# Optimization experiments

Measured on AMD Instinct MI355X. Metric: run time of the kernel, lower is better.

## Reference

```python
import jax, jax.numpy as jnp
import numpy as np

N_NODES = 10000
W_DIM = 512
N_EDGES = 200000


def setup_inputs() -> dict:
    key = jax.random.key(0)
    k1, k2, k3 = jax.random.split(key, 3)
    z_drug = jax.random.normal(k1, (N_NODES, W_DIM), dtype=jnp.float32)
    # glorot-style init for the bilinear weight
    glorot_std = jnp.sqrt(2.0 / (W_DIM + W_DIM)).astype(jnp.float32)
    weight = jax.random.normal(k2, (W_DIM, W_DIM), dtype=jnp.float32) * glorot_std
    batch_edges = jax.random.randint(k3, (2, N_EDGES), 0, N_NODES, dtype=jnp.int64)
    return {"z_drug": z_drug, "weight": weight, "batch_edges": batch_edges}


def reference(z_drug, weight, batch_edges):
    # edge_type == 'drug_drug': both endpoints come from the drug table.
    row_embed = z_drug[batch_edges[0]]  # [E, d]
    col_embed = z_drug[batch_edges[1]]  # [E, d]
    # score_e = row_e @ W @ col_e  == diag((Z1 W) Z2^T) without the N x N blowup
    score = jnp.einsum('ed,df,ef->e', row_embed, weight, col_embed)
    return jax.nn.sigmoid(score)  # is_sigmoid=True default
```

## Files before the change

kernel.cpp:

```cpp
#include <hip/hip_runtime.h>
#include <math.h>

#define DIM     512
#define NNODES  10000
#define NEDGES  200000
#define MPAD    10048
#define NMB     157
#define NGRP    5
#define NB      (NGRP * NNODES)
#define SCAN_BLK 49

using short8  = __attribute__((ext_vector_type(8))) short;
using floatx4 = __attribute__((ext_vector_type(4))) float;
using half8   = __attribute__((ext_vector_type(8))) _Float16;
using half2v  = __attribute__((ext_vector_type(2))) _Float16;

__device__ inline float dot2acc(half2v a, half2v b, float c) {
#if __has_builtin(__builtin_amdgcn_fdot2)
    return __builtin_amdgcn_fdot2(a, b, c, false);
#else
    return fmaf((float)a[0], (float)b[0], fmaf((float)a[1], (float)b[1], c));
#endif
}

#define PREP_ZBLK 2512
__global__ __launch_bounds__(256) void prep(const float* __restrict__ Z,
                                            const float* __restrict__ W,
                                            _Float16* __restrict__ Zh16,
                                            _Float16* __restrict__ Wh16t,
                                            int* __restrict__ counts) {
    const int b = blockIdx.x;
    const int t = threadIdx.x;

    if (b < 196) {
        int i = b * 256 + t;
        if (i < NB) counts[i] = 0;
    }

    if (b < PREP_ZBLK) {
        const int idx8 = (b * 256 + t) * 8;
        const int m = idx8 >> 9;
        float x[8];
        if (m < NNODES) {
            float4 v0 = *(const float4*)(Z + idx8);
            float4 v1 = *(const float4*)(Z + idx8 + 4);
            x[0]=v0.x; x[1]=v0.y; x[2]=v0.z; x[3]=v0.w;
            x[4]=v1.x; x[5]=v1.y; x[6]=v1.z; x[7]=v1.w;
        } else {
            #pragma unroll
            for (int j = 0; j < 8; ++j) x[j] = 0.f;
        }
        half8 h;
        #pragma unroll
        for (int j = 0; j < 8; ++j) h[j] = (_Float16)x[j];
        *(half8*)(Zh16 + idx8) = h;
    } else {
        __shared__ float tile[64][65];
        const int wb = b - PREP_ZBLK;
        const int kb = (wb >> 3) * 64;
        const int nb = (wb & 7) * 64;
        const int kk = t >> 2;
        const int ch = t & 3;

        const float* src = W + (size_t)(kb + kk) * DIM + nb + ch * 16;
        #pragma unroll
        for (int q = 0; q < 4; ++q) {
            float4 v = *(const float4*)(src + q * 4);
            tile[kk][ch * 16 + q * 4 + 0] = v.x;
            tile[kk][ch * 16 + q * 4 + 1] = v.y;
            tile[kk][ch * 16 + q * 4 + 2] = v.z;
            tile[kk][ch * 16 + q * 4 + 3] = v.w;
        }
        __syncthreads();

        const int nn = kk;
        half8 h0, h1;
        #pragma unroll
        for (int i = 0; i < 8; ++i) h0[i] = (_Float16)tile[ch * 16 + i][nn];
        #pragma unroll
        for (int i = 0; i < 8; ++i) h1[i] = (_Float16)tile[ch * 16 + 8 + i][nn];
        _Float16* d = Wh16t + (size_t)(nb + nn) * DIM + kb + ch * 16;
        *(half8*)(d)     = h0;
        *(half8*)(d + 8) = h1;
    }
}

__global__ __launch_bounds__(256) void gemm_f16(const _Float16* __restrict__ Zh16,
                                                const _Float16* __restrict__ Wh16t,
                                                _Float16* __restrict__ ZWh) {
    __shared__ _Float16 Abuf[2][64 * 32];
    __shared__ _Float16 Bbuf[2][128 * 32];

    const int t     = threadIdx.x;
    const int bid   = blockIdx.x;
    const int n_idx = bid & 3;
    const int m0    = (bid >> 2) * 64;
    const int n0    = n_idx * 128;

    const int l  = t & 63;
    const int w  = t >> 6;
    const int wn = w * 32;
    const int lm = l & 15;
    const int lq = l >> 4;
    const unsigned wbase = (unsigned)(t & 192);

    floatx4 acc[4][2] = {};

    const int arow = t >> 2;
    const int ach  = t & 3;

    auto stage = [&](int buf, int k0) {
        {
            const _Float16* s = Zh16 + (size_t)(m0 + arow) * DIM + k0 + ach * 8;
            __builtin_amdgcn_global_load_lds(
                (const __attribute__((address_space(1))) void*)s,
                (__attribute__((address_space(3))) void*)&Abuf[buf][wbase * 8], 16, 0, 0);
        }
        #pragma unroll
        for (int p = 0; p < 2; ++p) {
            const int sidx = p * 256 + t;
            const int row  = sidx >> 2;
            const int ch   = sidx & 3;
            const _Float16* s = Wh16t + (size_t)(n0 + row) * DIM + k0 + ch * 8;
            __builtin_amdgcn_global_load_lds(
                (const __attribute__((address_space(1))) void*)s,
                (__attribute__((address_space(3))) void*)&Bbuf[buf][(p * 256 + wbase) * 8], 16, 0, 0);
        }
    };

    stage(0, 0);
    __syncthreads();

    for (int s = 0; s < 16; ++s) {
        const int buf = s & 1;
        if (s < 15) stage(buf ^ 1, (s + 1) * 32);

        half8 aF[4], bF[2];
        #pragma unroll
        for (int i = 0; i < 4; ++i)
            aF[i] = *(const half8*)&Abuf[buf][(16 * i + lm) * 32 + lq * 8];
        #pragma unroll
        for (int j = 0; j < 2; ++j)
            bF[j] = *(const half8*)&Bbuf[buf][(wn + 16 * j + lm) * 32 + lq * 8];

        #pragma unroll
        for (int i = 0; i < 4; ++i)
            #pragma unroll
            for (int j = 0; j < 2; ++j)
                acc[i][j] = __builtin_amdgcn_mfma_f32_16x16x32_f16(aF[i], bF[j], acc[i][j], 0, 0, 0);

        __syncthreads();
    }

    #pragma unroll
    for (int i = 0; i < 4; ++i)
        #pragma unroll
        for (int j = 0; j < 2; ++j)
            #pragma unroll
            for (int r = 0; r < 4; ++r) {
                const int gm = m0 + 16 * i + lq * 4 + r;
                const int gn = n0 + wn + 16 * j + lm;
                if (gm < NNODES)
                    ZWh[(size_t)gm * DIM + gn] = (_Float16)acc[i][j][r];
            }
}

__global__ void hist_rows(const int* __restrict__ eidx, int* __restrict__ counts) {
    int e = blockIdx.x * blockDim.x + threadIdx.x;
    if (e < NEDGES) {
        int r = eidx[e];
        int c = eidx[NEDGES + e];
        atomicAdd(&counts[(c >> 11) * NNODES + r], 1);
    }
}

__global__ __launch_bounds__(1024) void scan_local(const int* __restrict__ counts,
                                                   int* __restrict__ partial,
                                                   int* __restrict__ blksum) {
    __shared__ int wsum[16];
    __shared__ int woff[17];
    const int t    = threadIdx.x;
    const int lane = t & 63;
    const int wv   = t >> 6;
    const int i    = blockIdx.x * 1024 + t;

    int x = (i < NB) ? counts[i] : 0;

    int v = x;
    #pragma unroll
    for (int off = 1; off < 64; off <<= 1) {
        int u = __shfl_up(v, off, 64);
        if (lane >= off) v += u;
    }
    if (lane == 63) wsum[wv] = v;
    __syncthreads();
    if (t == 0) {
        int r = 0;
        #pragma unroll
        for (int k = 0; k < 16; ++k) { woff[k] = r; r += wsum[k]; }
        woff[16] = r;
    }
    __syncthreads();

    if (i < NB) partial[i] = woff[wv] + (v - x);
    if (t == 1023) blksum[blockIdx.x] = woff[16];
}

__global__ __launch_bounds__(1024) void scan_fix(const int* __restrict__ counts,
                                                 const int* __restrict__ partial,
                                                 const int* __restrict__ blksum,
                                                 int* __restrict__ offs,
                                                 int* __restrict__ cursor) {
    __shared__ int base_s;
    const int t = threadIdx.x;
    const int b = blockIdx.x;

    if (t < 64) {
        int v = (t < b) ? blksum[t] : 0;
        #pragma unroll
        for (int off = 32; off > 0; off >>= 1)
            v += __shfl_xor(v, off, 64);
        if (t == 0) base_s = v;
    }
    __syncthreads();
    const int base = base_s;

    const int i = b * 1024 + t;
    if (i < NB) {
        int off = base + partial[i];
        offs[i]   = off;
        cursor[i] = off;
        if (i == NB - 1) offs[NB] = off + counts[i];
    }
}

__global__ void scatter_edges(const int* __restrict__ eidx,
                              int* __restrict__ cursor,
                              unsigned* __restrict__ keys) {
    int e = blockIdx.x * blockDim.x + threadIdx.x;
    if (e < NEDGES) {
        int r = eidx[e];
        int c = eidx[NEDGES + e];
        int pos = atomicAdd(&cursor[(c >> 11) * NNODES + r], 1);
        keys[pos] = ((unsigned)c << 18) | (unsigned)e;
    }
}

__global__ __launch_bounds__(256) void edge_score_q(const _Float16* __restrict__ ZWh,
                                                    const _Float16* __restrict__ Zh,
                                                    const unsigned* __restrict__ keys,
                                                    const int* __restrict__ offs,
                                                    float* __restrict__ out) {
    const int b = blockIdx.x * 4 + (threadIdx.x >> 6);
    const int start = offs[b];
    const int end   = offs[b + 1];
    if (start == end) return;

    const unsigned g = (unsigned)b / NNODES;
    const int r = b - (int)g * NNODES;

    const int lane = threadIdx.x & 63;
    const int gq   = lane >> 4;
    const int sl   = lane & 15;

    const _Float16* rp = ZWh + (size_t)r * DIM + sl * 32;
    half8 ra0 = *(const half8*)(rp);
    half8 ra1 = *(const half8*)(rp + 8);
    half8 ra2 = *(const half8*)(rp + 16);
    half8 ra3 = *(const half8*)(rp + 24);

    for (int i = start; i < end; i += 4) {
        const int ii = i + gq;
        const unsigned k = keys[ii < end ? ii : (end - 1)];
        const int c = (int)(k >> 18);

        const _Float16* cp = Zh + (size_t)c * DIM + sl * 32;
        half8 c0 = *(const half8*)(cp);
        half8 c1 = *(const half8*)(cp + 8);
        half8 c2 = *(const half8*)(cp + 16);
        half8 c3 = *(const half8*)(cp + 24);

        float s = 0.f;
        #pragma unroll
        for (int d = 0; d < 4; ++d) {
            s = dot2acc((half2v){ra0[2*d], ra0[2*d+1]}, (half2v){c0[2*d], c0[2*d+1]}, s);
            s = dot2acc((half2v){ra1[2*d], ra1[2*d+1]}, (half2v){c1[2*d], c1[2*d+1]}, s);
            s = dot2acc((half2v){ra2[2*d], ra2[2*d+1]}, (half2v){c2[2*d], c2[2*d+1]}, s);
            s = dot2acc((half2v){ra3[2*d], ra3[2*d+1]}, (half2v){c3[2*d], c3[2*d+1]}, s);
        }

        s += __shfl_xor(s, 1, 64);
        s += __shfl_xor(s, 2, 64);
        s += __shfl_xor(s, 4, 64);
        s += __shfl_xor(s, 8, 64);

        if (sl == 0 && ii < end)
            out[k & 0x3FFFFu] = 1.0f / (1.0f + expf(-s));
    }
}

#define GTM 128
#define GTN 64
#define GTK 16
#define LDA 132
#define LDB 68

__global__ __launch_bounds__(256) void gemm_zw(const float* __restrict__ A,
                                               const float* __restrict__ B,
                                               float* __restrict__ C) {
    __shared__ float As[GTK * LDA];
    __shared__ float Bs[GTK * LDB];

    const int t  = threadIdx.x;
    const int m0 = blockIdx.x * GTM;
    const int n0 = blockIdx.y * GTN;
    const int tx = t & 15;
    const int ty = t >> 4;

    float acc[8][4] = {};

    for (int k0 = 0; k0 < DIM; k0 += GTK) {
        #pragma unroll
        for (int p = 0; p < 2; ++p) {
            int f  = t + p * 256;
            int mm = f >> 2;
            int kq = f & 3;
            int m  = m0 + mm;
            float4 v = make_float4(0.f, 0.f, 0.f, 0.f);
            if (m < NNODES)
                v = *(const float4*)(A + (size_t)m * DIM + k0 + kq * 4);
            As[(kq * 4 + 0) * LDA + mm] = v.x;
            As[(kq * 4 + 1) * LDA + mm] = v.y;
            As[(kq * 4 + 2) * LDA + mm] = v.z;
            As[(kq * 4 + 3) * LDA + mm] = v.w;
        }
        {
            int kb = t >> 4, n4 = t & 15;
            *(float4*)&Bs[kb * LDB + n4 * 4] =
                *(const float4*)(B + (size_t)(k0 + kb) * DIM + n0 + n4 * 4);
        }
        __syncthreads();

        #pragma unroll
        for (int kk = 0; kk < GTK; ++kk) {
            float4 a0 = *(const float4*)&As[kk * LDA + ty * 8];
            float4 a1 = *(const float4*)&As[kk * LDA + ty * 8 + 4];
            float4 b  = *(const float4*)&Bs[kk * LDB + tx * 4];
            float av[8] = {a0.x, a0.y, a0.z, a0.w, a1.x, a1.y, a1.z, a1.w};
            float bv[4] = {b.x, b.y, b.z, b.w};
            #pragma unroll
            for (int i = 0; i < 8; ++i)
                #pragma unroll
                for (int j = 0; j < 4; ++j)
                    acc[i][j] = fmaf(av[i], bv[j], acc[i][j]);
        }
        __syncthreads();
    }

    #pragma unroll
    for (int i = 0; i < 8; ++i) {
        int m = m0 + ty * 8 + i;
        if (m < NNODES)
            *(float4*)(C + (size_t)m * DIM + n0 + tx * 4) =
                make_float4(acc[i][0], acc[i][1], acc[i][2], acc[i][3]);
    }
}

__global__ __launch_bounds__(256) void edge_score(const float* __restrict__ ZW,
                                                  const float* __restrict__ Z,
                                                  const int* __restrict__ eidx,
                                                  float* __restrict__ out) {
    const int e    = blockIdx.x * 4 + (threadIdx.x >> 6);
    const int lane = threadIdx.x & 63;

    const int r = eidx[e];
    const int c = eidx[NEDGES + e];

    const float4* pr = (const float4*)(ZW + (size_t)r * DIM);
    const float4* pc = (const float4*)(Z  + (size_t)c * DIM);

    float4 a0 = pr[lane * 2 + 0];
    float4 a1 = pr[lane * 2 + 1];
    float4 b0 = pc[lane * 2 + 0];
    float4 b1 = pc[lane * 2 + 1];

    float s = a0.x * b0.x;
    s = fmaf(a0.y, b0.y, s);
    s = fmaf(a0.z, b0.z, s);
    s = fmaf(a0.w, b0.w, s);
    s = fmaf(a1.x, b1.x, s);
    s = fmaf(a1.y, b1.y, s);
    s = fmaf(a1.z, b1.z, s);
    s = fmaf(a1.w, b1.w, s);

    #pragma unroll
    for (int off = 32; off > 0; off >>= 1)
        s += __shfl_xor(s, off, 64);

    if (lane == 0)
        out[e] = 1.0f / (1.0f + expf(-s));
}

extern "C" void kernel_launch(void* const* d_in, const int* in_sizes, int n_in,
                              void* d_out, int out_size, void* d_ws, size_t ws_size,
                              hipStream_t stream) {
    const float* Z  = (const float*)d_in[0];
    const float* W  = (const float*)d_in[1];
    const int*   EI = (const int*)d_in[2];
    float* out = (float*)d_out;

    char* p = (char*)d_ws;
    _Float16* ZWh   = (_Float16*)p;  p += (size_t)MPAD * DIM * 2;
    _Float16* Zh16  = (_Float16*)p;  p += (size_t)MPAD * DIM * 2;
    _Float16* Wh16t = (_Float16*)p;  p += (size_t)DIM * DIM * 2;
    int* counts  = (int*)p;          p += (size_t)NB * 4;
    int* offs    = (int*)p;          p += (size_t)(NB + 1) * 4;
    int* cursor  = (int*)p;          p += (size_t)NB * 4;
    int* partial = (int*)p;          p += (size_t)NB * 4;
    int* blksum  = (int*)p;          p += (size_t)SCAN_BLK * 4;
    unsigned* keys = (unsigned*)p;   p += (size_t)NEDGES * 4;
    const size_t need_full = (size_t)(p - (char*)d_ws);

    if (ws_size >= need_full) {
        prep<<<PREP_ZBLK + 64, 256, 0, stream>>>(Z, W, Zh16, Wh16t, counts);
        gemm_f16<<<NMB * 4, 256, 0, stream>>>(Zh16, Wh16t, ZWh);
        hist_rows<<<(NEDGES + 255) / 256, 256, 0, stream>>>(EI, counts);
        scan_local<<<SCAN_BLK, 1024, 0, stream>>>(counts, partial, blksum);
        scan_fix<<<SCAN_BLK, 1024, 0, stream>>>(counts, partial, blksum, offs, cursor);
        scatter_edges<<<(NEDGES + 255) / 256, 256, 0, stream>>>(EI, cursor, keys);
        edge_score_q<<<NB / 4, 256, 0, stream>>>(ZWh, Zh16, keys, offs, out);
    } else {
        float* ZW = (float*)d_ws;
        dim3 g1((NNODES + GTM - 1) / GTM, DIM / GTN);
        gemm_zw<<<g1, 256, 0, stream>>>(Z, W, ZW);
        edge_score<<<NEDGES / 4, 256, 0, stream>>>(ZW, Z, EI, out);
    }
}
```

Before: 142.8 us.

## Fuse edge counting, scan and scatter into one cooperative kernel

Replaces the four separate launches (histogram, two-pass scan, scatter) and the counts zeroing in prep with a single cooperative kernel of 196 blocks that uses grid-wide syncs between phases. This is meant to remove kernel launch gaps and per-launch overhead in the edge-bucketing pipeline. In exchange, only 196 blocks do the histogram and scatter work with grid-stride loops, and each grid.sync has its own cost. If the cooperative launch fails, it falls back to the old multi-kernel path.

```diff
diff --git a/kernel.cpp b/kernel.cpp
--- a/kernel.cpp
+++ b/kernel.cpp
@@ -1,5 +1,8 @@
 #include <hip/hip_runtime.h>
+#include <hip/hip_cooperative_groups.h>
 #include <math.h>
+
+namespace cg = cooperative_groups;
 
 #define DIM     512
 #define NNODES  10000
@@ -8,7 +11,7 @@
 #define NMB     157
 #define NGRP    5
 #define NB      (NGRP * NNODES)
-#define SCAN_BLK 49
+#define SORT_BLK 196
 
 using short8  = __attribute__((ext_vector_type(8))) short;
 using floatx4 = __attribute__((ext_vector_type(4))) float;
@@ -27,15 +30,9 @@
 __global__ __launch_bounds__(256) void prep(const float* __restrict__ Z,
                                             const float* __restrict__ W,
                                             _Float16* __restrict__ Zh16,
-                                            _Float16* __restrict__ Wh16t,
-                                            int* __restrict__ counts) {
+                                            _Float16* __restrict__ Wh16t) {
     const int b = blockIdx.x;
     const int t = threadIdx.x;
-
-    if (b < 196) {
-        int i = b * 256 + t;
-        if (i < NB) counts[i] = 0;
-    }
 
     if (b < PREP_ZBLK) {
         const int idx8 = (b * 256 + t) * 8;
@@ -165,6 +162,92 @@
             }
 }
 
+__global__ __launch_bounds__(256) void sort_all(const int* __restrict__ eidx,
+                                                int* __restrict__ counts,
+                                                int* __restrict__ partial,
+                                                int* __restrict__ blksum,
+                                                int* __restrict__ offs,
+                                                int* __restrict__ cursor,
+                                                unsigned* __restrict__ keys) {
+    cg::grid_group grid = cg::this_grid();
+    const int b = blockIdx.x;
+    const int t = threadIdx.x;
+    const int gt = b * 256 + t;
+    const int nthreads = SORT_BLK * 256;
+
+    if (gt < NB) counts[gt] = 0;
+    grid.sync();
+
+    for (int e = gt; e < NEDGES; e += nthreads) {
+        int r = eidx[e];
+        int c = eidx[NEDGES + e];
+        atomicAdd(&counts[(c >> 11) * NNODES + r], 1);
+    }
+    grid.sync();
+
+    {
+        __shared__ int wsum[4];
+        __shared__ int woff[5];
+        const int lane = t & 63;
+        const int wv   = t >> 6;
+
+        int x = (gt < NB) ? counts[gt] : 0;
+        int v = x;
+        #pragma unroll
+        for (int off = 1; off < 64; off <<= 1) {
+            int u = __shfl_up(v, off, 64);
+            if (lane >= off) v += u;
+        }
+        if (lane == 63) wsum[wv] = v;
+        __syncthreads();
+        if (t == 0) {
+            int r = 0;
+            #pragma unroll
+            for (int k = 0; k < 4; ++k) { woff[k] = r; r += wsum[k]; }
+            woff[4] = r;
+        }
+        __syncthreads();
+        if (gt < NB) partial[gt] = woff[wv] + (v - x);
+        if (t == 255) blksum[b] = woff[4];
+    }
+    grid.sync();
+
+    {
+        __shared__ int psum[4];
+        __shared__ int base_s;
+        const int lane = t & 63;
+        const int wv   = t >> 6;
+        int v = (t < b) ? blksum[t] : 0;
+        #pragma unroll
+        for (int off = 32; off > 0; off >>= 1)
+            v += __shfl_xor(v, off, 64);
+        if (lane == 0) psum[wv] = v;
+        __syncthreads();
+        if (t == 0) base_s = psum[0] + psum[1] + psum[2] + psum[3];
+        __syncthreads();
+        const int base = base_s;
+        if (gt < NB) {
+            int off = base + partial[gt];
+            offs[gt]   = off;
+            cursor[gt] = off;
+            if (gt == NB - 1) offs[NB] = off + counts[gt];
+        }
+    }
+    grid.sync();
+
+    for (int e = gt; e < NEDGES; e += nthreads) {
+        int r = eidx[e];
+        int c = eidx[NEDGES + e];
+        int pos = atomicAdd(&cursor[(c >> 11) * NNODES + r], 1);
+        keys[pos] = ((unsigned)c << 18) | (unsigned)e;
+    }
+}
+
+__global__ void zero_counts_k(int* __restrict__ counts) {
+    int i = blockIdx.x * blockDim.x + threadIdx.x;
+    if (i < NB) counts[i] = 0;
+}
+
 __global__ void hist_rows(const int* __restrict__ eidx, int* __restrict__ counts) {
     int e = blockIdx.x * blockDim.x + threadIdx.x;
     if (e < NEDGES) {
@@ -417,17 +500,27 @@
     int* offs    = (int*)p;          p += (size_t)(NB + 1) * 4;
     int* cursor  = (int*)p;          p += (size_t)NB * 4;
     int* partial = (int*)p;          p += (size_t)NB * 4;
-    int* blksum  = (int*)p;          p += (size_t)SCAN_BLK * 4;
+    int* blksum  = (int*)p;          p += (size_t)SORT_BLK * 4;
     unsigned* keys = (unsigned*)p;   p += (size_t)NEDGES * 4;
     const size_t need_full = (size_t)(p - (char*)d_ws);
 
     if (ws_size >= need_full) {
-        prep<<<PREP_ZBLK + 64, 256, 0, stream>>>(Z, W, Zh16, Wh16t, counts);
+        prep<<<PREP_ZBLK + 64, 256, 0, stream>>>(Z, W, Zh16, Wh16t);
         gemm_f16<<<NMB * 4, 256, 0, stream>>>(Zh16, Wh16t, ZWh);
-        hist_rows<<<(NEDGES + 255) / 256, 256, 0, stream>>>(EI, counts);
-        scan_local<<<SCAN_BLK, 1024, 0, stream>>>(counts, partial, blksum);
-        scan_fix<<<SCAN_BLK, 1024, 0, stream>>>(counts, partial, blksum, offs, cursor);
-        scatter_edges<<<(NEDGES + 255) / 256, 256, 0, stream>>>(EI, cursor, keys);
+
+        void* args[] = {(void*)&EI, (void*)&counts, (void*)&partial,
+                        (void*)&blksum, (void*)&offs, (void*)&cursor, (void*)&keys};
+        hipError_t err = hipLaunchCooperativeKernel(
+            reinterpret_cast<void*>(sort_all), dim3(SORT_BLK), dim3(256),
+            args, 0, stream);
+        if (err != hipSuccess) {
+            zero_counts_k<<<(NB + 255) / 256, 256, 0, stream>>>(counts);
+            hist_rows<<<(NEDGES + 255) / 256, 256, 0, stream>>>(EI, counts);
+            scan_local<<<49, 1024, 0, stream>>>(counts, partial, blksum);
+            scan_fix<<<49, 1024, 0, stream>>>(counts, partial, blksum, offs, cursor);
+            scatter_edges<<<(NEDGES + 255) / 256, 256, 0, stream>>>(EI, cursor, keys);
+        }
+
         edge_score_q<<<NB / 4, 256, 0, stream>>>(ZWh, Zh16, keys, offs, out);
     } else {
         float* ZW = (float*)d_ws;
```

New measurement: 234.6 us. +64.3%, slower.

## Flatten bucketed edge scoring to one edge per quarter-wave using sorted keys

Applied to the files above, without the earlier changes.

The scoring kernel no longer assigns one wave per (column-group, row) bucket and loops over its edges. Instead it launches a flat grid where each 16-lane group handles exactly one sorted edge, reading the row index from a new 16-bit array written during scatter. This removes load imbalance, idle waves on empty buckets, and the offsets array. In exchange the row vector of ZW is reloaded for every edge rather than once per bucket, relying on cache hits from the sorted order.

```diff
diff --git a/kernel.cpp b/kernel.cpp
--- a/kernel.cpp
+++ b/kernel.cpp
@@ -206,10 +206,8 @@
     if (t == 1023) blksum[blockIdx.x] = woff[16];
 }
 
-__global__ __launch_bounds__(1024) void scan_fix(const int* __restrict__ counts,
-                                                 const int* __restrict__ partial,
+__global__ __launch_bounds__(1024) void scan_fix(const int* __restrict__ partial,
                                                  const int* __restrict__ blksum,
-                                                 int* __restrict__ offs,
                                                  int* __restrict__ cursor) {
     __shared__ int base_s;
     const int t = threadIdx.x;
@@ -226,77 +224,68 @@
     const int base = base_s;
 
     const int i = b * 1024 + t;
-    if (i < NB) {
-        int off = base + partial[i];
-        offs[i]   = off;
-        cursor[i] = off;
-        if (i == NB - 1) offs[NB] = off + counts[i];
-    }
+    if (i < NB)
+        cursor[i] = base + partial[i];
 }
 
 __global__ void scatter_edges(const int* __restrict__ eidx,
                               int* __restrict__ cursor,
-                              unsigned* __restrict__ keys) {
+                              unsigned* __restrict__ keys,
+                              unsigned short* __restrict__ rows16) {
     int e = blockIdx.x * blockDim.x + threadIdx.x;
     if (e < NEDGES) {
         int r = eidx[e];
         int c = eidx[NEDGES + e];
         int pos = atomicAdd(&cursor[(c >> 11) * NNODES + r], 1);
-        keys[pos] = ((unsigned)c << 18) | (unsigned)e;
-    }
-}
-
-__global__ __launch_bounds__(256) void edge_score_q(const _Float16* __restrict__ ZWh,
+        keys[pos]   = ((unsigned)c << 18) | (unsigned)e;
+        rows16[pos] = (unsigned short)r;
+    }
+}
+
+__global__ __launch_bounds__(256) void edge_score_f(const _Float16* __restrict__ ZWh,
                                                     const _Float16* __restrict__ Zh,
                                                     const unsigned* __restrict__ keys,
-                                                    const int* __restrict__ offs,
+                                                    const unsigned short* __restrict__ rows16,
                                                     float* __restrict__ out) {
-    const int b = blockIdx.x * 4 + (threadIdx.x >> 6);
-    const int start = offs[b];
-    const int end   = offs[b + 1];
-    if (start == end) return;
-
-    const unsigned g = (unsigned)b / NNODES;
-    const int r = b - (int)g * NNODES;
-
-    const int lane = threadIdx.x & 63;
+    const int t    = threadIdx.x;
+    const int wgid = blockIdx.x * 4 + (t >> 6);
+    const int lane = t & 63;
     const int gq   = lane >> 4;
     const int sl   = lane & 15;
 
+    const int ii = wgid * 4 + gq;
+    const unsigned k = keys[ii];
+    const int c = (int)(k >> 18);
+    const int r = (int)rows16[ii];
+
     const _Float16* rp = ZWh + (size_t)r * DIM + sl * 32;
+    const _Float16* cp = Zh  + (size_t)c * DIM + sl * 32;
+
     half8 ra0 = *(const half8*)(rp);
     half8 ra1 = *(const half8*)(rp + 8);
     half8 ra2 = *(const half8*)(rp + 16);
     half8 ra3 = *(const half8*)(rp + 24);
-
-    for (int i = start; i < end; i += 4) {
-        const int ii = i + gq;
-        const unsigned k = keys[ii < end ? ii : (end - 1)];
-        const int c = (int)(k >> 18);
-
-        const _Float16* cp = Zh + (size_t)c * DIM + sl * 32;
-        half8 c0 = *(const half8*)(cp);
-        half8 c1 = *(const half8*)(cp + 8);
-        half8 c2 = *(const half8*)(cp + 16);
-        half8 c3 = *(const half8*)(cp + 24);
-
-        float s = 0.f;
-        #pragma unroll
-        for (int d = 0; d < 4; ++d) {
-            s = dot2acc((half2v){ra0[2*d], ra0[2*d+1]}, (half2v){c0[2*d], c0[2*d+1]}, s);
-            s = dot2acc((half2v){ra1[2*d], ra1[2*d+1]}, (half2v){c1[2*d], c1[2*d+1]}, s);
-            s = dot2acc((half2v){ra2[2*d], ra2[2*d+1]}, (half2v){c2[2*d], c2[2*d+1]}, s);
-            s = dot2acc((half2v){ra3[2*d], ra3[2*d+1]}, (half2v){c3[2*d], c3[2*d+1]}, s);
-        }
-
-        s += __shfl_xor(s, 1, 64);
-        s += __shfl_xor(s, 2, 64);
-        s += __shfl_xor(s, 4, 64);
-        s += __shfl_xor(s, 8, 64);
-
-        if (sl == 0 && ii < end)
-            out[k & 0x3FFFFu] = 1.0f / (1.0f + expf(-s));
-    }
+    half8 c0  = *(const half8*)(cp);
+    half8 c1  = *(const half8*)(cp + 8);
+    half8 c2  = *(const half8*)(cp + 16);
+    half8 c3  = *(const half8*)(cp + 24);
+
+    float s = 0.f;
+    #pragma unroll
+    for (int d = 0; d < 4; ++d) {
+        s = dot2acc((half2v){ra0[2*d], ra0[2*d+1]}, (half2v){c0[2*d], c0[2*d+1]}, s);
+        s = dot2acc((half2v){ra1[2*d], ra1[2*d+1]}, (half2v){c1[2*d], c1[2*d+1]}, s);
+        s = dot2acc((half2v){ra2[2*d], ra2[2*d+1]}, (half2v){c2[2*d], c2[2*d+1]}, s);
+        s = dot2acc((half2v){ra3[2*d], ra3[2*d+1]}, (half2v){c3[2*d], c3[2*d+1]}, s);
+    }
+
+    s += __shfl_xor(s, 1, 64);
+    s += __shfl_xor(s, 2, 64);
+    s += __shfl_xor(s, 4, 64);
+    s += __shfl_xor(s, 8, 64);
+
+    if (sl == 0)
+        out[k & 0x3FFFFu] = 1.0f / (1.0f + expf(-s));
 }
 
 #define GTM 128
@@ -414,11 +403,11 @@
     _Float16* Zh16  = (_Float16*)p;  p += (size_t)MPAD * DIM * 2;
     _Float16* Wh16t = (_Float16*)p;  p += (size_t)DIM * DIM * 2;
     int* counts  = (int*)p;          p += (size_t)NB * 4;
-    int* offs    = (int*)p;          p += (size_t)(NB + 1) * 4;
     int* cursor  = (int*)p;          p += (size_t)NB * 4;
     int* partial = (int*)p;          p += (size_t)NB * 4;
     int* blksum  = (int*)p;          p += (size_t)SCAN_BLK * 4;
     unsigned* keys = (unsigned*)p;   p += (size_t)NEDGES * 4;
+    unsigned short* rows16 = (unsigned short*)p; p += (size_t)NEDGES * 2;
     const size_t need_full = (size_t)(p - (char*)d_ws);
 
     if (ws_size >= need_full) {
@@ -426,9 +415,9 @@
         gemm_f16<<<NMB * 4, 256, 0, stream>>>(Zh16, Wh16t, ZWh);
         hist_rows<<<(NEDGES + 255) / 256, 256, 0, stream>>>(EI, counts);
         scan_local<<<SCAN_BLK, 1024, 0, stream>>>(counts, partial, blksum);
-        scan_fix<<<SCAN_BLK, 1024, 0, stream>>>(counts, partial, blksum, offs, cursor);
-        scatter_edges<<<(NEDGES + 255) / 256, 256, 0, stream>>>(EI, cursor, keys);
-        edge_score_q<<<NB / 4, 256, 0, stream>>>(ZWh, Zh16, keys, offs, out);
+        scan_fix<<<SCAN_BLK, 1024, 0, stream>>>(partial, blksum, cursor);
+        scatter_edges<<<(NEDGES + 255) / 256, 256, 0, stream>>>(EI, cursor, keys, rows16);
+        edge_score_f<<<NEDGES / 16, 256, 0, stream>>>(ZWh, Zh16, keys, rows16, out);
     } else {
         float* ZW = (float*)d_ws;
         dim3 g1((NNODES + GTM - 1) / GTM, DIM / GTN);
```

New measurement: 140.1 us. Within noise of the previous version (-1.9%).
